# Optimization experiments

Hardware: AMD Instinct MI355X
Metric: run time of the kernel (lower is better)

## Reference

```python
import jax, jax.numpy as jnp
import numpy as np

D_IN = 1024
D_OUT = 1024
NUM_HEADS = 16
HEAD_DIM = D_OUT // NUM_HEADS


def setup_inputs() -> dict:
    key = jax.random.key(0)
    ks = jax.random.split(key, 6)
    scale = 0.02
    x = jax.random.normal(ks[0], (2, 2048, D_IN), dtype=jnp.float32)
    Wq = jax.random.normal(ks[1], (D_IN, D_OUT), dtype=jnp.float32) * scale
    Wk = jax.random.normal(ks[2], (D_IN, D_OUT), dtype=jnp.float32) * scale
    Wv = jax.random.normal(ks[3], (D_IN, D_OUT), dtype=jnp.float32) * scale
    Wo = jax.random.normal(ks[4], (D_OUT, D_OUT), dtype=jnp.float32) * scale
    bo = jax.random.normal(ks[5], (D_OUT,), dtype=jnp.float32) * scale
    return {"x": x, "Wq": Wq, "Wk": Wk, "Wv": Wv, "Wo": Wo, "bo": bo}


def reference(x, Wq, Wk, Wv, Wo, bo):
    b, T, _ = x.shape
    h, dh = NUM_HEADS, HEAD_DIM
    # QKV projections (no bias), split heads: [b,T,d_out] -> [b,h,T,dh]
    q = (x @ Wq).reshape(b, T, h, dh).transpose(0, 2, 1, 3)
    k = (x @ Wk).reshape(b, T, h, dh).transpose(0, 2, 1, 3)
    v = (x @ Wv).reshape(b, T, h, dh).transpose(0, 2, 1, 3)
    # scaled dot-product scores with causal mask
    scores = jnp.einsum("bhqd,bhkd->bhqk", q, k) / jnp.sqrt(jnp.float32(dh))
    causal = jnp.tril(jnp.ones((T, T), dtype=bool))  # True = allowed
    scores = jnp.where(causal, scores, -jnp.inf)
    attn = jax.nn.softmax(scores, axis=-1)
    # dropout p=0.0 -> identity
    ctx = jnp.einsum("bhqk,bhkd->bhqd", attn, v)
    ctx = ctx.transpose(0, 2, 1, 3).reshape(b, T, h * dh)
    return ctx @ Wo + bo
```

## Files before the change

kernel.cpp:

```cpp
#include <hip/hip_runtime.h>

typedef __attribute__((ext_vector_type(8))) __bf16 bf16x8;
typedef __attribute__((ext_vector_type(4))) __bf16 bf16x4;
typedef __attribute__((ext_vector_type(4))) float  f32x4;

static constexpr int TSEQ    = 2048;
static constexpr int DMODEL  = 1024;
static constexpr int HD      = 64;
static constexpr int VSTRIDE = 2080;
static constexpr int LSTR    = 72;

#define AS1 __attribute__((address_space(1)))
#define AS3 __attribute__((address_space(3)))

__global__ __launch_bounds__(256) void k_prep(const float* __restrict__ x,
    const float* __restrict__ w0, const float* __restrict__ w1,
    const float* __restrict__ w2, const float* __restrict__ w3,
    __bf16* __restrict__ xbf, __bf16* __restrict__ wt_all) {
  __shared__ float tile[32][33];
  const int blk = blockIdx.x;
  const int tid = threadIdx.x;
  if (blk < 4096) {
    size_t i = ((size_t)blk * 256 + tid) * 4;
    float4 v = *(const float4*)(x + i);
    bf16x4 o = { (__bf16)v.x, (__bf16)v.y, (__bf16)v.z, (__bf16)v.w };
    *(bf16x4*)(xbf + i) = o;
    return;
  }
  const int tz = blk - 4096;
  const int wi = tz >> 10;
  const int tl = tz & 1023;
  const int n0 = (tl & 31) * 32, k0 = (tl >> 5) * 32;
  const float* w = wi == 0 ? w0 : wi == 1 ? w1 : wi == 2 ? w2 : w3;
  __bf16* out = wt_all + (size_t)wi * DMODEL * DMODEL;
  const int tx = tid & 31, ty0 = (tid >> 5) * 4;
#pragma unroll
  for (int j = 0; j < 4; j++)
    tile[ty0 + j][tx] = w[(size_t)(k0 + ty0 + j) * DMODEL + n0 + tx];
  __syncthreads();
#pragma unroll
  for (int j = 0; j < 4; j++)
    out[(size_t)(n0 + ty0 + j) * DMODEL + k0 + tx] = (__bf16)tile[tx][ty0 + j];
}

__device__ __forceinline__ void gemm_mainloop(const __bf16* __restrict__ A,
                                              const __bf16* __restrict__ Bt,
                                              int bm, int bn,
                                              __bf16* At, __bf16* Bl,
                                              f32x4 acc[4][4]) {
  const int tid  = threadIdx.x;
  const int lane = tid & 63;
  const int l15  = lane & 15, quad = lane >> 4;
  const int wv   = tid >> 6;
  const int wm   = (wv >> 1) * 64, wn = (wv & 1) * 64;
  const int s0   = wv * 2;
  const int srow = lane >> 2;
  const int scol = (lane & 3) << 3;
  for (int k0 = 0; k0 < 1024; k0 += 32) {
    __syncthreads();
#pragma unroll
    for (int ss = 0; ss < 2; ss++) {
      const int s   = s0 + ss;
      const int row = s * 16 + srow;
      const __bf16* ga = A  + (size_t)(bm + row) * 1024 + k0 + scol;
      const __bf16* gb = Bt + (size_t)(bn + row) * 1024 + k0 + scol;
      __builtin_amdgcn_global_load_lds((const AS1 void*)ga,
                                       (AS3 void*)(At + s * 512), 16, 0, 0);
      __builtin_amdgcn_global_load_lds((const AS1 void*)gb,
                                       (AS3 void*)(Bl + s * 512), 16, 0, 0);
    }
    __syncthreads();
    bf16x8 af[4], bfr[4];
#pragma unroll
    for (int mt = 0; mt < 4; mt++)
      af[mt] = *(const bf16x8*)(At + (wm + mt * 16 + l15) * 32 + quad * 8);
#pragma unroll
    for (int nt = 0; nt < 4; nt++)
      bfr[nt] = *(const bf16x8*)(Bl + (wn + nt * 16 + l15) * 32 + quad * 8);
#pragma unroll
    for (int mt = 0; mt < 4; mt++)
#pragma unroll
      for (int nt = 0; nt < 4; nt++)
        acc[mt][nt] = __builtin_amdgcn_mfma_f32_16x16x32_bf16(
            af[mt], bfr[nt], acc[mt][nt], 0, 0, 0);
  }
}

__global__ __launch_bounds__(256) void k_gemm_qkv(const __bf16* __restrict__ xbf,
    const __bf16* __restrict__ wt_all, __bf16* __restrict__ qws,
    __bf16* __restrict__ kws, __bf16* __restrict__ vtws) {
  __shared__ __bf16 At[128 * 32];
  __shared__ __bf16 Bl[128 * 32];
  const int which = blockIdx.z;
  const __bf16* wt = wt_all + (size_t)which * DMODEL * DMODEL;
  const int bm = blockIdx.y * 128, bn = blockIdx.x * 128;
  f32x4 acc[4][4];
  const f32x4 z = {0.f, 0.f, 0.f, 0.f};
#pragma unroll
  for (int mt = 0; mt < 4; mt++)
#pragma unroll
    for (int nt = 0; nt < 4; nt++) acc[mt][nt] = z;
  gemm_mainloop(xbf, wt, bm, bn, At, Bl, acc);
  const int lane = threadIdx.x & 63;
  const int l15 = lane & 15, quad = lane >> 4;
  const int wv = threadIdx.x >> 6;
  const int wm = (wv >> 1) * 64, wn = (wv & 1) * 64;
#pragma unroll
  for (int mt = 0; mt < 4; mt++)
#pragma unroll
    for (int nt = 0; nt < 4; nt++)
#pragma unroll
      for (int r = 0; r < 4; r++) {
        int m = bm + wm + mt * 16 + quad * 4 + r;
        int n = bn + wn + nt * 16 + l15;
        int b = m >> 11, t = m & 2047;
        int h = n >> 6,  d = n & 63;
        int bh = b * 16 + h;
        float av = acc[mt][nt][r];
        if (which == 0)      qws[((size_t)bh * TSEQ + t) * HD + d] = (__bf16)(av * 0.125f);
        else if (which == 1) kws[((size_t)bh * TSEQ + t) * HD + d] = (__bf16)av;
        else                 vtws[((size_t)bh * HD + d) * VSTRIDE + t] = (__bf16)av;
      }
}

__global__ __launch_bounds__(256) void k_attn(const __bf16* __restrict__ qws,
    const __bf16* __restrict__ kws, const __bf16* __restrict__ vtws,
    __bf16* __restrict__ ctx) {
  const int bh  = blockIdx.x & 31;
  const int qb0 = blockIdx.x >> 5, qb1 = 31 - qb0;
  const int tid = threadIdx.x;
  const int lane = tid & 63, wv = tid >> 6;
  const int l15 = lane & 15, quad = lane >> 4;
  const __bf16* qp = qws  + (size_t)bh * TSEQ * HD;
  const __bf16* kp = kws  + (size_t)bh * TSEQ * HD;
  const __bf16* vp = vtws + (size_t)bh * HD * VSTRIDE;
  const int b = bh >> 4, h = bh & 15;

  __shared__ __bf16 kbuf[2][64 * LSTR];
  __shared__ __bf16 vbuf[2][64 * LSTR];
  __shared__ __bf16 plds[4][16 * LSTR];

  const f32x4 z = {0.f, 0.f, 0.f, 0.f};
  const int sr = tid >> 3, sc = (tid & 7) * 8;

  const int qr0a = qb0 * 64 + wv * 16;
  const int qr0b = qb1 * 64 + wv * 16;
  bf16x8 aq0[2], aq1[2];
#pragma unroll
  for (int kb = 0; kb < 2; kb++) {
    aq0[kb] = *(const bf16x8*)(qp + (size_t)(qr0a + l15) * HD + kb * 32 + quad * 8);
    aq1[kb] = *(const bf16x8*)(qp + (size_t)(qr0b + l15) * HD + kb * 32 + quad * 8);
  }

  bf16x8 kreg[2], vreg[2];
  kreg[0] = *(const bf16x8*)(kp + (size_t)sr * HD + sc);
  kreg[1] = *(const bf16x8*)(kp + (size_t)(sr + 32) * HD + sc);
  vreg[0] = *(const bf16x8*)(vp + (size_t)sr * VSTRIDE + sc);
  vreg[1] = *(const bf16x8*)(vp + (size_t)(sr + 32) * VSTRIDE + sc);
  *(bf16x8*)(kbuf[0] + sr * LSTR + sc)        = kreg[0];
  *(bf16x8*)(kbuf[0] + (sr + 32) * LSTR + sc) = kreg[1];
  *(bf16x8*)(vbuf[0] + sr * LSTR + sc)        = vreg[0];
  *(bf16x8*)(vbuf[0] + (sr + 32) * LSTR + sc) = vreg[1];
  __syncthreads();

  float lpart[4] = {0.f, 0.f, 0.f, 0.f};
  f32x4 acc[4];
#pragma unroll
  for (int dt = 0; dt < 4; dt++) acc[dt] = z;

  for (int s = 0; s < 33; s++) {
    const int cur = s & 1;
    const bool h0 = (s <= qb0);
    const bool masked = (s == qb0) || (s == 32);

    if (s + 1 < 33) {
      const int ktn = (s + 1 <= qb0) ? (s + 1) * 64 : (s - qb0) * 64;
      kreg[0] = *(const bf16x8*)(kp + (size_t)(ktn + sr) * HD + sc);
      kreg[1] = *(const bf16x8*)(kp + (size_t)(ktn + sr + 32) * HD + sc);
      vreg[0] = *(const bf16x8*)(vp + (size_t)sr * VSTRIDE + ktn + sc);
      vreg[1] = *(const bf16x8*)(vp + (size_t)(sr + 32) * VSTRIDE + ktn + sc);
    }

    const __bf16* kb_ = kbuf[cur];
    const __bf16* vb_ = vbuf[cur];
    f32x4 sarr[4];
#pragma unroll
    for (int nt = 0; nt < 4; nt++) sarr[nt] = z;
#pragma unroll
    for (int nt = 0; nt < 4; nt++)
#pragma unroll
      for (int kb = 0; kb < 2; kb++) {
        bf16x8 bk = *(const bf16x8*)(kb_ + (nt * 16 + l15) * LSTR + kb * 32 + quad * 8);
        bf16x8 a  = h0 ? aq0[kb] : aq1[kb];
        sarr[nt] = __builtin_amdgcn_mfma_f32_16x16x32_bf16(a, bk, sarr[nt], 0, 0, 0);
      }
    if (masked) {
#pragma unroll
      for (int r = 0; r < 4; r++) {
        const int qloc = wv * 16 + quad * 4 + r;
#pragma unroll
        for (int nt = 0; nt < 4; nt++) {
          int kloc = nt * 16 + l15;
          float p = (kloc <= qloc) ? __expf(sarr[nt][r]) : 0.f;
          lpart[r] += p;
          plds[wv][(quad * 4 + r) * LSTR + nt * 16 + l15] = (__bf16)p;
        }
      }
    } else {
#pragma unroll
      for (int r = 0; r < 4; r++)
#pragma unroll
        for (int nt = 0; nt < 4; nt++) {
          float p = __expf(sarr[nt][r]);
          lpart[r] += p;
          plds[wv][(quad * 4 + r) * LSTR + nt * 16 + l15] = (__bf16)p;
        }
    }
#pragma unroll
    for (int kb = 0; kb < 2; kb++) {
      bf16x8 ap = *(const bf16x8*)(&plds[wv][l15 * LSTR + kb * 32 + quad * 8]);
#pragma unroll
      for (int dt = 0; dt < 4; dt++) {
        bf16x8 bvv = *(const bf16x8*)(vb_ + (dt * 16 + l15) * LSTR + kb * 32 + quad * 8);
        acc[dt] = __builtin_amdgcn_mfma_f32_16x16x32_bf16(ap, bvv, acc[dt], 0, 0, 0);
      }
    }

    if (s + 1 < 33) {
      const int nxt = cur ^ 1;
      *(bf16x8*)(kbuf[nxt] + sr * LSTR + sc)        = kreg[0];
      *(bf16x8*)(kbuf[nxt] + (sr + 32) * LSTR + sc) = kreg[1];
      *(bf16x8*)(vbuf[nxt] + sr * LSTR + sc)        = vreg[0];
      *(bf16x8*)(vbuf[nxt] + (sr + 32) * LSTR + sc) = vreg[1];
    }
    __syncthreads();

    if (masked) {
      const int qr0 = h0 ? qr0a : qr0b;
#pragma unroll
      for (int r = 0; r < 4; r++) {
        float l = lpart[r];
        l += __shfl_xor(l, 1, 64);
        l += __shfl_xor(l, 2, 64);
        l += __shfl_xor(l, 4, 64);
        l += __shfl_xor(l, 8, 64);
        float linv = 1.f / l;
        const int qrow = qr0 + quad * 4 + r;
#pragma unroll
        for (int dt = 0; dt < 4; dt++)
          ctx[((size_t)(b * TSEQ + qrow)) * DMODEL + h * 64 + dt * 16 + l15] =
              (__bf16)(acc[dt][r] * linv);
        lpart[r] = 0.f;
      }
#pragma unroll
      for (int dt = 0; dt < 4; dt++) acc[dt] = z;
    }
  }
}

__global__ __launch_bounds__(256) void k_gemm_out(const __bf16* __restrict__ ctx,
    const __bf16* __restrict__ wot, const float* __restrict__ bo,
    float* __restrict__ out) {
  __shared__ __bf16 At[128 * 32];
  __shared__ __bf16 Bl[128 * 32];
  const int bm = blockIdx.y * 128, bn = blockIdx.x * 128;
  f32x4 acc[4][4];
  const f32x4 z = {0.f, 0.f, 0.f, 0.f};
#pragma unroll
  for (int mt = 0; mt < 4; mt++)
#pragma unroll
    for (int nt = 0; nt < 4; nt++) acc[mt][nt] = z;
  gemm_mainloop(ctx, wot, bm, bn, At, Bl, acc);
  const int lane = threadIdx.x & 63;
  const int l15 = lane & 15, quad = lane >> 4;
  const int wv = threadIdx.x >> 6;
  const int wm = (wv >> 1) * 64, wn = (wv & 1) * 64;
#pragma unroll
  for (int mt = 0; mt < 4; mt++)
#pragma unroll
    for (int nt = 0; nt < 4; nt++)
#pragma unroll
      for (int r = 0; r < 4; r++) {
        int m = bm + wm + mt * 16 + quad * 4 + r;
        int n = bn + wn + nt * 16 + l15;
        out[(size_t)m * DMODEL + n] = acc[mt][nt][r] + bo[n];
      }
}

extern "C" void kernel_launch(void* const* d_in, const int* in_sizes, int n_in,
                              void* d_out, int out_size, void* d_ws, size_t ws_size,
                              hipStream_t stream) {
  const float* x  = (const float*)d_in[0];
  const float* Wq = (const float*)d_in[1];
  const float* Wk = (const float*)d_in[2];
  const float* Wv = (const float*)d_in[3];
  const float* Wo = (const float*)d_in[4];
  const float* bo = (const float*)d_in[5];
  float* out = (float*)d_out;

  __bf16* xbf  = (__bf16*)d_ws;
  __bf16* wt   = xbf  + (size_t)4096 * 1024;
  __bf16* qws  = wt   + (size_t)4 * 1024 * 1024;
  __bf16* kws  = qws  + (size_t)32 * 2048 * 64;
  __bf16* vtws = kws  + (size_t)32 * 2048 * 64;
  __bf16* ctx  = xbf;

  k_prep<<<8192, 256, 0, stream>>>(x, Wq, Wk, Wv, Wo, xbf, wt);
  k_gemm_qkv<<<dim3(8, 32, 3), 256, 0, stream>>>(xbf, wt, qws, kws, vtws);
  k_attn<<<512, 256, 0, stream>>>(qws, kws, vtws, ctx);
  k_gemm_out<<<dim3(8, 32), 256, 0, stream>>>(ctx, wt + (size_t)3 * 1024 * 1024, bo, out);
}
```

Before: 190.9 us.

## Share K/V tiles across paired query blocks and use exp2 with folded log2e

```diff
diff --git a/kernel.cpp b/kernel.cpp
--- a/kernel.cpp
+++ b/kernel.cpp
@@ -12,6 +12,10 @@
 
 #define AS1 __attribute__((address_space(1)))
 #define AS3 __attribute__((address_space(3)))
+
+__device__ __forceinline__ float fast_exp2(float x) {
+  return __builtin_amdgcn_exp2f(x);
+}
 
 __global__ __launch_bounds__(256) void k_prep(const float* __restrict__ x,
     const float* __restrict__ w0, const float* __restrict__ w1,
@@ -117,7 +121,7 @@
         int h = n >> 6,  d = n & 63;
         int bh = b * 16 + h;
         float av = acc[mt][nt][r];
-        if (which == 0)      qws[((size_t)bh * TSEQ + t) * HD + d] = (__bf16)(av * 0.125f);
+        if (which == 0)      qws[((size_t)bh * TSEQ + t) * HD + d] = (__bf16)(av * 0.18033688f);
         else if (which == 1) kws[((size_t)bh * TSEQ + t) * HD + d] = (__bf16)av;
         else                 vtws[((size_t)bh * HD + d) * VSTRIDE + t] = (__bf16)av;
       }
@@ -126,8 +130,11 @@
 __global__ __launch_bounds__(256) void k_attn(const __bf16* __restrict__ qws,
     const __bf16* __restrict__ kws, const __bf16* __restrict__ vtws,
     __bf16* __restrict__ ctx) {
-  const int bh  = blockIdx.x & 31;
-  const int qb0 = blockIdx.x >> 5, qb1 = 31 - qb0;
+  const int blk  = blockIdx.x;
+  const int bh   = blk & 31;
+  const int qidx = blk >> 5;
+  const int qb0  = qidx < 8 ? qidx : 23 - qidx;
+  const int qb1  = 31 - qb0;
   const int tid = threadIdx.x;
   const int lane = tid & 63, wv = tid >> 6;
   const int l15 = lane & 15, quad = lane >> 4;
@@ -138,72 +145,104 @@
 
   __shared__ __bf16 kbuf[2][64 * LSTR];
   __shared__ __bf16 vbuf[2][64 * LSTR];
-  __shared__ __bf16 plds[4][16 * LSTR];
+  __shared__ __bf16 pldsa[4][16 * LSTR];
+  __shared__ __bf16 pldsb[4][16 * LSTR];
 
   const f32x4 z = {0.f, 0.f, 0.f, 0.f};
   const int sr = tid >> 3, sc = (tid & 7) * 8;
 
   const int qr0a = qb0 * 64 + wv * 16;
   const int qr0b = qb1 * 64 + wv * 16;
-  bf16x8 aq0[2], aq1[2];
+  bf16x8 aqa[2], aqb[2];
 #pragma unroll
   for (int kb = 0; kb < 2; kb++) {
-    aq0[kb] = *(const bf16x8*)(qp + (size_t)(qr0a + l15) * HD + kb * 32 + quad * 8);
-    aq1[kb] = *(const bf16x8*)(qp + (size_t)(qr0b + l15) * HD + kb * 32 + quad * 8);
+    aqa[kb] = *(const bf16x8*)(qp + (size_t)(qr0a + l15) * HD + kb * 32 + quad * 8);
+    aqb[kb] = *(const bf16x8*)(qp + (size_t)(qr0b + l15) * HD + kb * 32 + quad * 8);
   }
 
   bf16x8 kreg[2], vreg[2];
-  kreg[0] = *(const bf16x8*)(kp + (size_t)sr * HD + sc);
-  kreg[1] = *(const bf16x8*)(kp + (size_t)(sr + 32) * HD + sc);
-  vreg[0] = *(const bf16x8*)(vp + (size_t)sr * VSTRIDE + sc);
-  vreg[1] = *(const bf16x8*)(vp + (size_t)(sr + 32) * VSTRIDE + sc);
-  *(bf16x8*)(kbuf[0] + sr * LSTR + sc)        = kreg[0];
-  *(bf16x8*)(kbuf[0] + (sr + 32) * LSTR + sc) = kreg[1];
-  *(bf16x8*)(vbuf[0] + sr * LSTR + sc)        = vreg[0];
-  *(bf16x8*)(vbuf[0] + (sr + 32) * LSTR + sc) = vreg[1];
+  auto load_tile = [&](int s) {
+    const int kt = s * 64;
+    kreg[0] = *(const bf16x8*)(kp + (size_t)(kt + sr) * HD + sc);
+    kreg[1] = *(const bf16x8*)(kp + (size_t)(kt + sr + 32) * HD + sc);
+    vreg[0] = *(const bf16x8*)(vp + (size_t)sr * VSTRIDE + kt + sc);
+    vreg[1] = *(const bf16x8*)(vp + (size_t)(sr + 32) * VSTRIDE + kt + sc);
+  };
+  auto store_tile = [&](int buf) {
+    *(bf16x8*)(kbuf[buf] + sr * LSTR + sc)        = kreg[0];
+    *(bf16x8*)(kbuf[buf] + (sr + 32) * LSTR + sc) = kreg[1];
+    *(bf16x8*)(vbuf[buf] + sr * LSTR + sc)        = vreg[0];
+    *(bf16x8*)(vbuf[buf] + (sr + 32) * LSTR + sc) = vreg[1];
+  };
+
+  float lpa[4] = {0.f, 0.f, 0.f, 0.f};
+  float lpb[4] = {0.f, 0.f, 0.f, 0.f};
+  f32x4 acca[4], accb[4];
+#pragma unroll
+  for (int dt = 0; dt < 4; dt++) { acca[dt] = z; accb[dt] = z; }
+
+  auto finalize = [&](float* lp, f32x4* acc, int qr0) {
+#pragma unroll
+    for (int r = 0; r < 4; r++) {
+      float l = lp[r];
+      l += __shfl_xor(l, 1, 64);
+      l += __shfl_xor(l, 2, 64);
+      l += __shfl_xor(l, 4, 64);
+      l += __shfl_xor(l, 8, 64);
+      float linv = 1.f / l;
+      const int qrow = qr0 + quad * 4 + r;
+#pragma unroll
+      for (int dt = 0; dt < 4; dt++)
+        ctx[((size_t)(b * TSEQ + qrow)) * DMODEL + h * 64 + dt * 16 + l15] =
+            (__bf16)(acc[dt][r] * linv);
+    }
+  };
+
+  load_tile(0);
+  store_tile(0);
   __syncthreads();
 
-  float lpart[4] = {0.f, 0.f, 0.f, 0.f};
-  f32x4 acc[4];
-#pragma unroll
-  for (int dt = 0; dt < 4; dt++) acc[dt] = z;
-
-  for (int s = 0; s < 33; s++) {
+  for (int s = 0; s <= qb1; s++) {
     const int cur = s & 1;
-    const bool h0 = (s <= qb0);
-    const bool masked = (s == qb0) || (s == 32);
-
-    if (s + 1 < 33) {
-      const int ktn = (s + 1 <= qb0) ? (s + 1) * 64 : (s - qb0) * 64;
-      kreg[0] = *(const bf16x8*)(kp + (size_t)(ktn + sr) * HD + sc);
-      kreg[1] = *(const bf16x8*)(kp + (size_t)(ktn + sr + 32) * HD + sc);
-      vreg[0] = *(const bf16x8*)(vp + (size_t)sr * VSTRIDE + ktn + sc);
-      vreg[1] = *(const bf16x8*)(vp + (size_t)(sr + 32) * VSTRIDE + ktn + sc);
-    }
+    const bool dual = (s <= qb0);
+
+    if (s + 1 <= qb1) load_tile(s + 1);
 
     const __bf16* kb_ = kbuf[cur];
     const __bf16* vb_ = vbuf[cur];
-    f32x4 sarr[4];
-#pragma unroll
-    for (int nt = 0; nt < 4; nt++) sarr[nt] = z;
-#pragma unroll
-    for (int nt = 0; nt < 4; nt++)
-#pragma unroll
-      for (int kb = 0; kb < 2; kb++) {
-        bf16x8 bk = *(const bf16x8*)(kb_ + (nt * 16 + l15) * LSTR + kb * 32 + quad * 8);
-        bf16x8 a  = h0 ? aq0[kb] : aq1[kb];
-        sarr[nt] = __builtin_amdgcn_mfma_f32_16x16x32_bf16(a, bk, sarr[nt], 0, 0, 0);
-      }
-    if (masked) {
+    f32x4 sa[4], sb[4];
+#pragma unroll
+    for (int nt = 0; nt < 4; nt++) { sb[nt] = z; sa[nt] = z; }
+
+    if (dual) {
+#pragma unroll
+      for (int nt = 0; nt < 4; nt++)
+#pragma unroll
+        for (int kb = 0; kb < 2; kb++) {
+          bf16x8 bk = *(const bf16x8*)(kb_ + (nt * 16 + l15) * LSTR + kb * 32 + quad * 8);
+          sb[nt] = __builtin_amdgcn_mfma_f32_16x16x32_bf16(aqb[kb], bk, sb[nt], 0, 0, 0);
+          sa[nt] = __builtin_amdgcn_mfma_f32_16x16x32_bf16(aqa[kb], bk, sa[nt], 0, 0, 0);
+        }
+    } else {
+#pragma unroll
+      for (int nt = 0; nt < 4; nt++)
+#pragma unroll
+        for (int kb = 0; kb < 2; kb++) {
+          bf16x8 bk = *(const bf16x8*)(kb_ + (nt * 16 + l15) * LSTR + kb * 32 + quad * 8);
+          sb[nt] = __builtin_amdgcn_mfma_f32_16x16x32_bf16(aqb[kb], bk, sb[nt], 0, 0, 0);
+        }
+    }
+
+    if (s == qb1) {
 #pragma unroll
       for (int r = 0; r < 4; r++) {
         const int qloc = wv * 16 + quad * 4 + r;
 #pragma unroll
         for (int nt = 0; nt < 4; nt++) {
           int kloc = nt * 16 + l15;
-          float p = (kloc <= qloc) ? __expf(sarr[nt][r]) : 0.f;
-          lpart[r] += p;
-          plds[wv][(quad * 4 + r) * LSTR + nt * 16 + l15] = (__bf16)p;
+          float p = (kloc <= qloc) ? fast_exp2(sb[nt][r]) : 0.f;
+          lpb[r] += p;
+          pldsb[wv][(quad * 4 + r) * LSTR + nt * 16 + l15] = (__bf16)p;
         }
       }
     } else {
@@ -211,51 +250,65 @@
       for (int r = 0; r < 4; r++)
 #pragma unroll
         for (int nt = 0; nt < 4; nt++) {
-          float p = __expf(sarr[nt][r]);
-          lpart[r] += p;
-          plds[wv][(quad * 4 + r) * LSTR + nt * 16 + l15] = (__bf16)p;
-        }
-    }
-#pragma unroll
-    for (int kb = 0; kb < 2; kb++) {
-      bf16x8 ap = *(const bf16x8*)(&plds[wv][l15 * LSTR + kb * 32 + quad * 8]);
-#pragma unroll
-      for (int dt = 0; dt < 4; dt++) {
-        bf16x8 bvv = *(const bf16x8*)(vb_ + (dt * 16 + l15) * LSTR + kb * 32 + quad * 8);
-        acc[dt] = __builtin_amdgcn_mfma_f32_16x16x32_bf16(ap, bvv, acc[dt], 0, 0, 0);
-      }
-    }
-
-    if (s + 1 < 33) {
-      const int nxt = cur ^ 1;
-      *(bf16x8*)(kbuf[nxt] + sr * LSTR + sc)        = kreg[0];
-      *(bf16x8*)(kbuf[nxt] + (sr + 32) * LSTR + sc) = kreg[1];
-      *(bf16x8*)(vbuf[nxt] + sr * LSTR + sc)        = vreg[0];
-      *(bf16x8*)(vbuf[nxt] + (sr + 32) * LSTR + sc) = vreg[1];
-    }
+          float p = fast_exp2(sb[nt][r]);
+          lpb[r] += p;
+          pldsb[wv][(quad * 4 + r) * LSTR + nt * 16 + l15] = (__bf16)p;
+        }
+    }
+    if (dual) {
+      if (s == qb0) {
+#pragma unroll
+        for (int r = 0; r < 4; r++) {
+          const int qloc = wv * 16 + quad * 4 + r;
+#pragma unroll
+          for (int nt = 0; nt < 4; nt++) {
+            int kloc = nt * 16 + l15;
+            float p = (kloc <= qloc) ? fast_exp2(sa[nt][r]) : 0.f;
+            lpa[r] += p;
+            pldsa[wv][(quad * 4 + r) * LSTR + nt * 16 + l15] = (__bf16)p;
+          }
+        }
+      } else {
+#pragma unroll
+        for (int r = 0; r < 4; r++)
+#pragma unroll
+          for (int nt = 0; nt < 4; nt++) {
+            float p = fast_exp2(sa[nt][r]);
+            lpa[r] += p;
+            pldsa[wv][(quad * 4 + r) * LSTR + nt * 16 + l15] = (__bf16)p;
+          }
+      }
+    }
+
+    if (dual) {
+#pragma unroll
+      for (int kb = 0; kb < 2; kb++) {
+        bf16x8 apb = *(const bf16x8*)(&pldsb[wv][l15 * LSTR + kb * 32 + quad * 8]);
+        bf16x8 apa = *(const bf16x8*)(&pldsa[wv][l15 * LSTR + kb * 32 + quad * 8]);
+#pragma unroll
+        for (int dt = 0; dt < 4; dt++) {
+          bf16x8 bvv = *(const bf16x8*)(vb_ + (dt * 16 + l15) * LSTR + kb * 32 + quad * 8);
+          accb[dt] = __builtin_amdgcn_mfma_f32_16x16x32_bf16(apb, bvv, accb[dt], 0, 0, 0);
+          acca[dt] = __builtin_amdgcn_mfma_f32_16x16x32_bf16(apa, bvv, acca[dt], 0, 0, 0);
+        }
+      }
+    } else {
+#pragma unroll
+      for (int kb = 0; kb < 2; kb++) {
+        bf16x8 apb = *(const bf16x8*)(&pldsb[wv][l15 * LSTR + kb * 32 + quad * 8]);
+#pragma unroll
+        for (int dt = 0; dt < 4; dt++) {
+          bf16x8 bvv = *(const bf16x8*)(vb_ + (dt * 16 + l15) * LSTR + kb * 32 + quad * 8);
+          accb[dt] = __builtin_amdgcn_mfma_f32_16x16x32_bf16(apb, bvv, accb[dt], 0, 0, 0);
+        }
+      }
+    }
+
+    if (s + 1 <= qb1) store_tile(cur ^ 1);
     __syncthreads();
-
-    if (masked) {
-      const int qr0 = h0 ? qr0a : qr0b;
-#pragma unroll
-      for (int r = 0; r < 4; r++) {
-        float l = lpart[r];
-        l += __shfl_xor(l, 1, 64);
-        l += __shfl_xor(l, 2, 64);
-        l += __shfl_xor(l, 4, 64);
-        l += __shfl_xor(l, 8, 64);
-        float linv = 1.f / l;
-        const int qrow = qr0 + quad * 4 + r;
-#pragma unroll
-        for (int dt = 0; dt < 4; dt++)
-          ctx[((size_t)(b * TSEQ + qrow)) * DMODEL + h * 64 + dt * 16 + l15] =
-              (__bf16)(acc[dt][r] * linv);
-        lpart[r] = 0.f;
-      }
-#pragma unroll
-      for (int dt = 0; dt < 4; dt++) acc[dt] = z;
-    }
+    if (s == qb0) finalize(lpa, acca, qr0a);
   }
+  finalize(lpb, accb, qr0b);
 }
 
 __global__ __launch_bounds__(256) void k_gemm_out(const __bf16* __restrict__ ctx,
```

Measured after the change: 192.2 us. No clear change (+0.7%).
